# Optimization experiments

Hardware: AMD Instinct MI355X
Metric: run time of the kernel (lower is better)

The kernel has to match this reference:

```python
import jax, jax.numpy as jnp
import numpy as np

NUM_TOKENS = 16384
HIDDEN = 4096
NUM_EXPERTS = 256
TOP_K = 8
N_GROUP = 8
TOPK_GROUP = 4
NORM_TOPK_PROB = True
ROUTED_SCALING_FACTOR = 1.0


def setup_inputs() -> dict:
    key = jax.random.key(0)
    k1, k2, k3 = jax.random.split(key, 3)
    hidden_states = jax.random.normal(k1, (NUM_TOKENS, HIDDEN), dtype=jnp.float32)
    weight = jax.random.normal(k2, (NUM_EXPERTS, HIDDEN), dtype=jnp.float32) * (HIDDEN ** -0.5)
    e_score_correction_bias = jax.random.normal(k3, (NUM_EXPERTS,), dtype=jnp.float32) * 0.01
    return {"hidden_states": hidden_states, "weight": weight,
            "e_score_correction_bias": e_score_correction_bias}


def reference(hidden_states, weight, e_score_correction_bias):
    num_tokens = hidden_states.shape[0]
    # router logits: [T, E]
    logits = jnp.einsum('th,eh->te', hidden_states.astype(jnp.float32),
                        weight.astype(jnp.float32))
    scores = jax.nn.sigmoid(logits)
    scores_for_choice = scores + e_score_correction_bias[None, :]
    # group scores: sum of top-2 within each group, [T, G]
    per_group = scores_for_choice.reshape(num_tokens, N_GROUP, NUM_EXPERTS // N_GROUP)
    top2_vals, _ = jax.lax.top_k(per_group, 2)
    group_scores = top2_vals.sum(axis=-1)
    # select topk_group groups, build mask over experts
    _, group_idx = jax.lax.top_k(group_scores, TOPK_GROUP)  # [T, topk_group]
    group_mask = jnp.zeros_like(group_scores).at[
        jnp.arange(num_tokens)[:, None], group_idx].set(1.0)  # [T, G]
    score_mask = jnp.repeat(group_mask, NUM_EXPERTS // N_GROUP, axis=1)  # [T, E]
    tmp_scores = jnp.where(score_mask > 0, scores_for_choice, -jnp.inf)
    # final top-k experts over masked scores
    _, topk_idx = jax.lax.top_k(tmp_scores, TOP_K)  # [T, K]
    topk_weight = jnp.take_along_axis(scores, topk_idx, axis=1)
    if TOP_K > 1 and NORM_TOPK_PROB:
        denom = topk_weight.sum(axis=-1, keepdims=True) + 1e-20
        topk_weight = topk_weight / denom
    topk_weight = topk_weight * ROUTED_SCALING_FACTOR
    return logits, topk_weight, topk_idx
```

## Files before the change

kernel.cpp:

```cpp
#include <hip/hip_runtime.h>
#include <hip/hip_bf16.h>
#include <math.h>

#define TKN 16384
#define HID 4096
#define NE  256
#define TOPK 8
#define NGRP 8
#define TOPG 4

#define BM 128
#define BK 64
#define NKT (HID / BK)
#define BIMG 32768

typedef _Float16 half8 __attribute__((ext_vector_type(8)));
typedef float    f32x4 __attribute__((ext_vector_type(4)));

static __device__ __forceinline__ unsigned pkrtz(float x, float y) {
    auto r = __builtin_amdgcn_cvt_pkrtz(x, y);
    return __builtin_bit_cast(unsigned, r);
}
static __device__ __forceinline__ float hi_mask(float a) {
    return __uint_as_float(__float_as_uint(a) & 0xFFFFE000u);
}

__global__ __launch_bounds__(256) void prep_b(const float* __restrict__ B,
                                              unsigned char* __restrict__ ws)
{
    const int gid = blockIdx.x * 256 + threadIdx.x;
    const int e   = gid >> 9;
    const int k0  = (gid & 511) * 8;
    const float* src = B + (size_t)e * HID + k0;
    float v[8];
    #pragma unroll
    for (int i = 0; i < 8; ++i) v[i] = src[i];
    unsigned hw[4], lw[4];
    #pragma unroll
    for (int j = 0; j < 4; ++j) {
        const float x0 = v[2*j], x1 = v[2*j+1];
        const float h0 = hi_mask(x0), h1 = hi_mask(x1);
        hw[j] = pkrtz(h0, h1);
        lw[j] = pkrtz(x0 - h0, x1 - h1);
    }
    const int cb     = e >> 7;
    const int row    = e & 127;
    const int rowgrp = row >> 4;
    const int lane16 = row & 15;
    const int kt     = k0 >> 6;
    const int kk     = k0 & 63;
    const int wg     = kk >> 5;
    const int kseg   = (kk >> 3) & 3;
    const int idx16  = ((rowgrp * 2 + wg) * 4 + kseg) * 16 + lane16;
    unsigned char* img = ws + (size_t)(cb * NKT + kt) * BIMG + idx16 * 16;
    *(uint4*)(img)         = make_uint4(hw[0], hw[1], hw[2], hw[3]);
    *(uint4*)(img + 16384) = make_uint4(lw[0], lw[1], lw[2], lw[3]);
}

__global__ __launch_bounds__(1024, 4) void gemm_mfma(
    const float* __restrict__ A, const unsigned char* __restrict__ Bws,
    float* __restrict__ C)
{
    __shared__ __align__(16) unsigned char smem[2][2][16384];

    const int tid  = threadIdx.x;
    const int lane = tid & 63;
    const int wave = tid >> 6;
    const int wg = wave >> 3;
    const int wr = (wave >> 2) & 1;
    const int wc = wave & 3;

    const int bid  = blockIdx.x;
    const int mb   = (bid & 7) * 16 + (bid >> 4);
    const int cb   = (bid >> 3) & 1;
    const int row0 = mb * BM;

    const int arow = tid >> 3;
    const int aseg = (tid & 7) * 8;
    const float* aG = A + (size_t)(row0 + arow) * HID + aseg;
    const int awx = arow * 128 + ((aseg * 2) ^ ((arow & 7) << 4));

    const int kx    = ((wg * 64) + ((lane >> 4) << 4)) ^ ((lane & 7) << 4);
    const int aRowB = (wr * 64 + (lane & 15)) * 128;

    const unsigned char* bBase = Bws + (size_t)cb * NKT * BIMG;
    const int boffH0 = ((wc * 2 + 0) * 2 + wg) * 1024 + lane * 16;
    const int boffH1 = ((wc * 2 + 1) * 2 + wg) * 1024 + lane * 16;

    f32x4 acc[4][2];
    #pragma unroll
    for (int i = 0; i < 4; ++i) { acc[i][0] = (f32x4)0.f; acc[i][1] = (f32x4)0.f; }

    float4 v0, v1;
    half8 bC[4], bN[4];

    v0 = *(const float4*)(aG);
    v1 = *(const float4*)(aG + 4);
    bC[0] = *(const half8*)(bBase + boffH0);
    bC[1] = *(const half8*)(bBase + 16384 + boffH0);
    bC[2] = *(const half8*)(bBase + boffH1);
    bC[3] = *(const half8*)(bBase + 16384 + boffH1);
    {
        const float h0 = hi_mask(v0.x), h1 = hi_mask(v0.y),
                    h2 = hi_mask(v0.z), h3 = hi_mask(v0.w);
        const float h4 = hi_mask(v1.x), h5 = hi_mask(v1.y),
                    h6 = hi_mask(v1.z), h7 = hi_mask(v1.w);
        *(uint4*)&smem[0][0][awx] = make_uint4(pkrtz(h0, h1), pkrtz(h2, h3),
                                               pkrtz(h4, h5), pkrtz(h6, h7));
        *(uint4*)&smem[0][1][awx] = make_uint4(pkrtz(v0.x - h0, v0.y - h1),
                                               pkrtz(v0.z - h2, v0.w - h3),
                                               pkrtz(v1.x - h4, v1.y - h5),
                                               pkrtz(v1.z - h6, v1.w - h7));
    }
    __syncthreads();

#define GSTEP(KT, BCUR, BNXT)                                                  \
    {                                                                          \
        const int kt_ = (KT);                                                  \
        const unsigned char* ub = &smem[kt_ & 1][0][0];                        \
        const bool more = (kt_ != NKT - 1);                                    \
        if (more) {                  \
            v0 = *(const float4*)(aG + (kt_ + 1) * BK);                        \
            v1 = *(const float4*)(aG + (kt_ + 1) * BK + 4);                    \
            const unsigned char* bp = bBase + (size_t)(kt_ + 1) * BIMG;        \
            BNXT[0] = *(const half8*)(bp + boffH0);                            \
            BNXT[1] = *(const half8*)(bp + 16384 + boffH0);                    \
            BNXT[2] = *(const half8*)(bp + boffH1);                            \
            BNXT[3] = *(const half8*)(bp + 16384 + boffH1);                    \
        }                                                                      \
        __builtin_amdgcn_sched_barrier(0);                                     \
        _Pragma("unroll")                                                      \
        for (int mt = 0; mt < 4; ++mt) {                                       \
            const half8 ah = *(const half8*)(ub + aRowB + mt * 2048 + kx);     \
            const half8 al = *(const half8*)(ub + 16384 + aRowB + mt * 2048 + kx); \
            f32x4 c0 = acc[mt][0];                                             \
            c0 = __builtin_amdgcn_mfma_f32_16x16x32_f16(ah, BCUR[0], c0, 0, 0, 0); \
            c0 = __builtin_amdgcn_mfma_f32_16x16x32_f16(ah, BCUR[1], c0, 0, 0, 0); \
            c0 = __builtin_amdgcn_mfma_f32_16x16x32_f16(al, BCUR[0], c0, 0, 0, 0); \
            acc[mt][0] = c0;                                                   \
            f32x4 c1 = acc[mt][1];                                             \
            c1 = __builtin_amdgcn_mfma_f32_16x16x32_f16(ah, BCUR[2], c1, 0, 0, 0); \
            c1 = __builtin_amdgcn_mfma_f32_16x16x32_f16(ah, BCUR[3], c1, 0, 0, 0); \
            c1 = __builtin_amdgcn_mfma_f32_16x16x32_f16(al, BCUR[2], c1, 0, 0, 0); \
            acc[mt][1] = c1;                                                   \
        }                                                                      \
        if (more) {        \
            const int nb = (kt_ + 1) & 1;                                      \
            const float h0 = hi_mask(v0.x), h1 = hi_mask(v0.y),                \
                        h2 = hi_mask(v0.z), h3 = hi_mask(v0.w);                \
            const float h4 = hi_mask(v1.x), h5 = hi_mask(v1.y),                \
                        h6 = hi_mask(v1.z), h7 = hi_mask(v1.w);                \
            *(uint4*)&smem[nb][0][awx] = make_uint4(pkrtz(h0, h1), pkrtz(h2, h3), \
                                                    pkrtz(h4, h5), pkrtz(h6, h7)); \
            *(uint4*)&smem[nb][1][awx] = make_uint4(pkrtz(v0.x - h0, v0.y - h1), \
                                                    pkrtz(v0.z - h2, v0.w - h3), \
                                                    pkrtz(v1.x - h4, v1.y - h5), \
                                                    pkrtz(v1.z - h6, v1.w - h7)); \
        }                                                                      \
        __syncthreads();                                                       \
    }

    for (int kt = 0; kt < NKT; kt += 2) {
        GSTEP(kt, bC, bN);
        GSTEP(kt + 1, bN, bC);
    }
#undef GSTEP

    float* redf = (float*)&smem[0][0][0];
    const int fb = (wave & 7) * 2048 + lane * 4;
    if (wg == 1) {
        #pragma unroll
        for (int mt = 0; mt < 4; ++mt)
            #pragma unroll
            for (int nt = 0; nt < 2; ++nt)
                *(f32x4*)&redf[fb + (mt * 2 + nt) * 256] = acc[mt][nt];
    }
    __syncthreads();
    if (wg == 0) {
        #pragma unroll
        for (int mt = 0; mt < 4; ++mt) {
            #pragma unroll
            for (int nt = 0; nt < 2; ++nt) {
                f32x4 o = acc[mt][nt] + *(const f32x4*)&redf[fb + (mt * 2 + nt) * 256];
                const int r0 = row0 + wr * 64 + mt * 16 + (lane >> 4) * 4;
                const int cc = cb * 128 + wc * 32 + nt * 16 + (lane & 15);
                #pragma unroll
                for (int r = 0; r < 4; ++r)
                    C[(size_t)(r0 + r) * NE + cc] = o[r];
            }
        }
    }
}

__global__ __launch_bounds__(256) void router_topk_kernel(
    const float* __restrict__ logits, const float* __restrict__ bias,
    float* __restrict__ out_w, float* __restrict__ out_i)
{
    const int wid  = threadIdx.x >> 6;
    const int lane = threadIdx.x & 63;
    const int token = blockIdx.x * 4 + wid;

    const float* row = logits + (size_t)token * NE;
    const float4 lg = *(const float4*)&row[lane * 4];

    float sig[4], sc[4];
    {
        const float l4[4] = {lg.x, lg.y, lg.z, lg.w};
        #pragma unroll
        for (int j = 0; j < 4; ++j) {
            sig[j] = 1.f / (1.f + expf(-l4[j]));
            sc[j]  = sig[j] + bias[lane * 4 + j];
        }
    }

    float m1 = sc[0], m2 = -INFINITY;
    #pragma unroll
    for (int j = 1; j < 4; ++j) {
        if (sc[j] > m1) { m2 = m1; m1 = sc[j]; }
        else if (sc[j] > m2) { m2 = sc[j]; }
    }
    #pragma unroll
    for (int off = 1; off < 8; off <<= 1) {
        const float o1 = __shfl_xor(m1, off);
        const float o2 = __shfl_xor(m2, off);
        const float lo = fminf(m1, o1);
        m1 = fmaxf(m1, o1);
        m2 = fmaxf(lo, fmaxf(m2, o2));
    }
    const float gscore = m1 + m2;

    const int gmy = lane >> 3;
    int rank = 0;
    #pragma unroll
    for (int g = 0; g < NGRP; ++g) {
        const float gs = __shfl(gscore, g * 8);
        if (gs > gscore || (gs == gscore && g < gmy)) ++rank;
    }
    if (rank >= TOPG) {
        #pragma unroll
        for (int j = 0; j < 4; ++j) sc[j] = -INFINITY;
    }

    float wk[TOPK]; int ik[TOPK];
    float wsum = 0.f;
    #pragma unroll
    for (int k = 0; k < TOPK; ++k) {
        float bv = sc[0]; int bi = lane * 4;
        #pragma unroll
        for (int j = 1; j < 4; ++j)
            if (sc[j] > bv) { bv = sc[j]; bi = lane * 4 + j; }
        #pragma unroll
        for (int off = 1; off < 64; off <<= 1) {
            const float v2 = __shfl_xor(bv, off);
            const int   i2 = __shfl_xor(bi, off);
            if (v2 > bv || (v2 == bv && i2 < bi)) { bv = v2; bi = i2; }
        }
        const int owner = bi >> 2;
        const int j = bi & 3;
        const float sv = (j == 0) ? sig[0] : (j == 1) ? sig[1] : (j == 2) ? sig[2] : sig[3];
        const float w = __shfl(sv, owner);
        wk[k] = w; ik[k] = bi; wsum += w;
        if (lane == owner) {
            if (j == 0) sc[0] = -INFINITY;
            else if (j == 1) sc[1] = -INFINITY;
            else if (j == 2) sc[2] = -INFINITY;
            else sc[3] = -INFINITY;
        }
    }

    if (lane == 0) {
        const float denom = wsum + 1e-20f;
        #pragma unroll
        for (int k = 0; k < TOPK; ++k) {
            out_w[(size_t)token * TOPK + k] = wk[k] / denom;
            out_i[(size_t)token * TOPK + k] = (float)ik[k];
        }
    }
}

extern "C" void kernel_launch(void* const* d_in, const int* in_sizes, int n_in,
                              void* d_out, int out_size, void* d_ws, size_t ws_size,
                              hipStream_t stream) {
    const float* hidden = (const float*)d_in[0];
    const float* weight = (const float*)d_in[1];
    const float* bias   = (const float*)d_in[2];

    float* logits = (float*)d_out;
    float* out_w  = logits + (size_t)TKN * NE;
    float* out_i  = out_w + (size_t)TKN * TOPK;

    unsigned char* bpl = (unsigned char*)d_ws;

    prep_b<<<512, 256, 0, stream>>>(weight, bpl);
    gemm_mfma<<<256, 1024, 0, stream>>>(hidden, bpl, logits);
    router_topk_kernel<<<TKN / 4, 256, 0, stream>>>(logits, bias, out_w, out_i);
}
```

Baseline: 165.0 us.

## Shrink GEMM column tile to 64 experts with 512-thread blocks

Reduces the GEMM block tile from 128x128 to 128x64 experts. Blocks now have 512 threads (8 waves split into two K-halves), and the grid grows to 512 blocks, re-mapped so blocks sharing A rows sit close together. The prepacked B image layout is reworked to match the 64-column tile, and each thread now loads and splits 16 A floats per K step. The aim is more blocks per GPU for better CU fill, at the cost of each A tile being re-read and re-split four times instead of twice.

Measured after the change: 171.8 us. 1.04x slower.

```diff
diff --git a/kernel.cpp b/kernel.cpp
--- a/kernel.cpp
+++ b/kernel.cpp
@@ -10,9 +10,10 @@
 #define TOPG 4
 
 #define BM 128
+#define BN 64
 #define BK 64
 #define NKT (HID / BK)
-#define BIMG 32768
+#define BIMG 16384
 
 typedef _Float16 half8 __attribute__((ext_vector_type(8)));
 typedef float    f32x4 __attribute__((ext_vector_type(4)));
@@ -43,21 +44,21 @@
         hw[j] = pkrtz(h0, h1);
         lw[j] = pkrtz(x0 - h0, x1 - h1);
     }
-    const int cb     = e >> 7;
-    const int row    = e & 127;
-    const int rowgrp = row >> 4;
-    const int lane16 = row & 15;
+    const int cb     = e >> 6;
+    const int colgrp = (e & 63) >> 4;
+    const int lane16 = e & 15;
     const int kt     = k0 >> 6;
     const int kk     = k0 & 63;
     const int wg     = kk >> 5;
     const int kseg   = (kk >> 3) & 3;
-    const int idx16  = ((rowgrp * 2 + wg) * 4 + kseg) * 16 + lane16;
-    unsigned char* img = ws + (size_t)(cb * NKT + kt) * BIMG + idx16 * 16;
-    *(uint4*)(img)         = make_uint4(hw[0], hw[1], hw[2], hw[3]);
-    *(uint4*)(img + 16384) = make_uint4(lw[0], lw[1], lw[2], lw[3]);
-}
-
-__global__ __launch_bounds__(1024, 4) void gemm_mfma(
+    const int f      = colgrp * 2 + wg;
+    unsigned char* img = ws + (size_t)(cb * NKT + kt) * BIMG
+                            + f * 2048 + (kseg * 16 + lane16) * 16;
+    *(uint4*)(img)        = make_uint4(hw[0], hw[1], hw[2], hw[3]);
+    *(uint4*)(img + 1024) = make_uint4(lw[0], lw[1], lw[2], lw[3]);
+}
+
+__global__ __launch_bounds__(512, 4) void gemm_mfma(
     const float* __restrict__ A, const unsigned char* __restrict__ Bws,
     float* __restrict__ C)
 {
@@ -66,51 +67,56 @@
     const int tid  = threadIdx.x;
     const int lane = tid & 63;
     const int wave = tid >> 6;
-    const int wg = wave >> 3;
-    const int wr = (wave >> 2) & 1;
-    const int wc = wave & 3;
-
-    const int bid  = blockIdx.x;
-    const int mb   = (bid & 7) * 16 + (bid >> 4);
-    const int cb   = (bid >> 3) & 1;
+    const int wg = wave >> 2;
+    const int wr = (wave >> 1) & 1;
+    const int wc = wave & 1;
+
+    const int logical = (blockIdx.x & 7) * 64 + (blockIdx.x >> 3);
+    const int mb   = logical >> 2;
+    const int cb   = logical & 3;
     const int row0 = mb * BM;
 
-    const int arow = tid >> 3;
-    const int aseg = (tid & 7) * 8;
+    const int arow = tid >> 2;
+    const int aseg = (tid & 3) * 16;
     const float* aG = A + (size_t)(row0 + arow) * HID + aseg;
-    const int awx = arow * 128 + ((aseg * 2) ^ ((arow & 7) << 4));
+    const int xorw = (arow & 7) << 4;
+    const int awx0 = arow * 128 + ((aseg * 2) ^ xorw);
+    const int awx1 = arow * 128 + ((aseg * 2 + 16) ^ xorw);
 
     const int kx    = ((wg * 64) + ((lane >> 4) << 4)) ^ ((lane & 7) << 4);
     const int aRowB = (wr * 64 + (lane & 15)) * 128;
 
     const unsigned char* bBase = Bws + (size_t)cb * NKT * BIMG;
-    const int boffH0 = ((wc * 2 + 0) * 2 + wg) * 1024 + lane * 16;
-    const int boffH1 = ((wc * 2 + 1) * 2 + wg) * 1024 + lane * 16;
+    const int f0off = ((wc * 2 + 0) * 2 + wg) * 2048 + lane * 16;
+    const int f1off = ((wc * 2 + 1) * 2 + wg) * 2048 + lane * 16;
 
     f32x4 acc[4][2];
     #pragma unroll
     for (int i = 0; i < 4; ++i) { acc[i][0] = (f32x4)0.f; acc[i][1] = (f32x4)0.f; }
 
-    float4 v0, v1;
+    float4 av[4];
     half8 bC[4], bN[4];
 
-    v0 = *(const float4*)(aG);
-    v1 = *(const float4*)(aG + 4);
-    bC[0] = *(const half8*)(bBase + boffH0);
-    bC[1] = *(const half8*)(bBase + 16384 + boffH0);
-    bC[2] = *(const half8*)(bBase + boffH1);
-    bC[3] = *(const half8*)(bBase + 16384 + boffH1);
+    #pragma unroll
+    for (int i = 0; i < 4; ++i) av[i] = *(const float4*)(aG + i * 4);
+    bC[0] = *(const half8*)(bBase + f0off);
+    bC[1] = *(const half8*)(bBase + f0off + 1024);
+    bC[2] = *(const half8*)(bBase + f1off);
+    bC[3] = *(const half8*)(bBase + f1off + 1024);
     {
-        const float h0 = hi_mask(v0.x), h1 = hi_mask(v0.y),
-                    h2 = hi_mask(v0.z), h3 = hi_mask(v0.w);
-        const float h4 = hi_mask(v1.x), h5 = hi_mask(v1.y),
-                    h6 = hi_mask(v1.z), h7 = hi_mask(v1.w);
-        *(uint4*)&smem[0][0][awx] = make_uint4(pkrtz(h0, h1), pkrtz(h2, h3),
-                                               pkrtz(h4, h5), pkrtz(h6, h7));
-        *(uint4*)&smem[0][1][awx] = make_uint4(pkrtz(v0.x - h0, v0.y - h1),
-                                               pkrtz(v0.z - h2, v0.w - h3),
-                                               pkrtz(v1.x - h4, v1.y - h5),
-                                               pkrtz(v1.z - h6, v1.w - h7));
+        unsigned hw[8], lw[8];
+        const float f[16] = {av[0].x,av[0].y,av[0].z,av[0].w, av[1].x,av[1].y,av[1].z,av[1].w,
+                             av[2].x,av[2].y,av[2].z,av[2].w, av[3].x,av[3].y,av[3].z,av[3].w};
+        #pragma unroll
+        for (int j = 0; j < 8; ++j) {
+            const float h0 = hi_mask(f[2*j]), h1 = hi_mask(f[2*j+1]);
+            hw[j] = pkrtz(h0, h1);
+            lw[j] = pkrtz(f[2*j] - h0, f[2*j+1] - h1);
+        }
+        *(uint4*)&smem[0][0][awx0] = make_uint4(hw[0], hw[1], hw[2], hw[3]);
+        *(uint4*)&smem[0][0][awx1] = make_uint4(hw[4], hw[5], hw[6], hw[7]);
+        *(uint4*)&smem[0][1][awx0] = make_uint4(lw[0], lw[1], lw[2], lw[3]);
+        *(uint4*)&smem[0][1][awx1] = make_uint4(lw[4], lw[5], lw[6], lw[7]);
     }
     __syncthreads();
 
@@ -119,14 +125,17 @@
         const int kt_ = (KT);                                                  \
         const unsigned char* ub = &smem[kt_ & 1][0][0];                        \
         const bool more = (kt_ != NKT - 1);                                    \
-        if (more) {                  \
-            v0 = *(const float4*)(aG + (kt_ + 1) * BK);                        \
-            v1 = *(const float4*)(aG + (kt_ + 1) * BK + 4);                    \
+        if (more) {                    \
+            const float* ap = aG + (kt_ + 1) * BK;                             \
+            av[0] = *(const float4*)(ap);                                      \
+            av[1] = *(const float4*)(ap + 4);                                  \
+            av[2] = *(const float4*)(ap + 8);                                  \
+            av[3] = *(const float4*)(ap + 12);                                 \
             const unsigned char* bp = bBase + (size_t)(kt_ + 1) * BIMG;        \
-            BNXT[0] = *(const half8*)(bp + boffH0);                            \
-            BNXT[1] = *(const half8*)(bp + 16384 + boffH0);                    \
-            BNXT[2] = *(const half8*)(bp + boffH1);                            \
-            BNXT[3] = *(const half8*)(bp + 16384 + boffH1);                    \
+            BNXT[0] = *(const half8*)(bp + f0off);                             \
+            BNXT[1] = *(const half8*)(bp + f0off + 1024);                      \
+            BNXT[2] = *(const half8*)(bp + f1off);                             \
+            BNXT[3] = *(const half8*)(bp + f1off + 1024);                      \
         }                                                                      \
         __builtin_amdgcn_sched_barrier(0);                                     \
         _Pragma("unroll")                                                      \
@@ -146,28 +155,33 @@
         }                                                                      \
         if (more) {        \
             const int nb = (kt_ + 1) & 1;                                      \
-            const float h0 = hi_mask(v0.x), h1 = hi_mask(v0.y),                \
-                        h2 = hi_mask(v0.z), h3 = hi_mask(v0.w);                \
-            const float h4 = hi_mask(v1.x), h5 = hi_mask(v1.y),                \
-                        h6 = hi_mask(v1.z), h7 = hi_mask(v1.w);                \
-            *(uint4*)&smem[nb][0][awx] = make_uint4(pkrtz(h0, h1), pkrtz(h2, h3), \
-                                                    pkrtz(h4, h5), pkrtz(h6, h7)); \
-            *(uint4*)&smem[nb][1][awx] = make_uint4(pkrtz(v0.x - h0, v0.y - h1), \
-                                                    pkrtz(v0.z - h2, v0.w - h3), \
-                                                    pkrtz(v1.x - h4, v1.y - h5), \
-                                                    pkrtz(v1.z - h6, v1.w - h7)); \
+            unsigned hw[8], lw[8];                                             \
+            const float f[16] = {av[0].x,av[0].y,av[0].z,av[0].w,              \
+                                 av[1].x,av[1].y,av[1].z,av[1].w,              \
+                                 av[2].x,av[2].y,av[2].z,av[2].w,              \
+                                 av[3].x,av[3].y,av[3].z,av[3].w};             \
+            _Pragma("unroll")                                                  \
+            for (int j = 0; j < 8; ++j) {                                      \
+                const float h0 = hi_mask(f[2*j]), h1 = hi_mask(f[2*j+1]);      \
+                hw[j] = pkrtz(h0, h1);                                         \
+                lw[j] = pkrtz(f[2*j] - h0, f[2*j+1] - h1);                     \
+            }                                                                  \
+            *(uint4*)&smem[nb][0][awx0] = make_uint4(hw[0], hw[1], hw[2], hw[3]); \
+            *(uint4*)&smem[nb][0][awx1] = make_uint4(hw[4], hw[5], hw[6], hw[7]); \
+            *(uint4*)&smem[nb][1][awx0] = make_uint4(lw[0], lw[1], lw[2], lw[3]); \
+            *(uint4*)&smem[nb][1][awx1] = make_uint4(lw[4], lw[5], lw[6], lw[7]); \
         }                                                                      \
         __syncthreads();                                                       \
     }
 
     for (int kt = 0; kt < NKT; kt += 2) {
-        GSTEP(kt, bC, bN);
+        GSTEP(kt,     bC, bN);
         GSTEP(kt + 1, bN, bC);
     }
 #undef GSTEP
 
     float* redf = (float*)&smem[0][0][0];
-    const int fb = (wave & 7) * 2048 + lane * 4;
+    const int fb = (wave & 3) * 2048 + lane * 4;
     if (wg == 1) {
         #pragma unroll
         for (int mt = 0; mt < 4; ++mt)
@@ -183,7 +197,7 @@
             for (int nt = 0; nt < 2; ++nt) {
                 f32x4 o = acc[mt][nt] + *(const f32x4*)&redf[fb + (mt * 2 + nt) * 256];
                 const int r0 = row0 + wr * 64 + mt * 16 + (lane >> 4) * 4;
-                const int cc = cb * 128 + wc * 32 + nt * 16 + (lane & 15);
+                const int cc = cb * BN + wc * 32 + nt * 16 + (lane & 15);
                 #pragma unroll
                 for (int r = 0; r < 4; ++r)
                     C[(size_t)(r0 + r) * NE + cc] = o[r];
@@ -292,6 +306,6 @@
     unsigned char* bpl = (unsigned char*)d_ws;
 
     prep_b<<<512, 256, 0, stream>>>(weight, bpl);
-    gemm_mfma<<<256, 1024, 0, stream>>>(hidden, bpl, logits);
+    gemm_mfma<<<512, 512, 0, stream>>>(hidden, bpl, logits);
     router_topk_kernel<<<TKN / 4, 256, 0, stream>>>(logits, bias, out_w, out_i);
 }
```
